# Performance work log

Measured on AMD Instinct MI355X. Metric: run time of the kernel, lower is better.

Reference implementation:

```python
import jax, jax.numpy as jnp
import numpy as np
from math import sqrt

EMA_W = 0.3  # ema_weight
LN_EPS = 1e-5


def setup_inputs() -> dict:
    key = jax.random.key(0)
    ks = jax.random.split(key, 16)
    B, L, H, E = 8, 1024, 8, 64
    d_ff, dp_rank = 2048, 8
    inp = {
        "queries": jax.random.normal(ks[0], (B, L, H, E), jnp.float32),
        "keys": jax.random.normal(ks[1], (B, L, H, E), jnp.float32),
        "values": jax.random.normal(ks[2], (B, L, H, E), jnp.float32),
        "attn_mask": jnp.zeros((B, 1, L, L), jnp.bool_),
        # dynamic-projection mlp: Linear(E, dp_rank)
        "mlp_w": jax.random.normal(ks[3], (E, dp_rank), jnp.float32) / sqrt(E),
        "mlp_b": jnp.zeros((dp_rank,), jnp.float32),
        # ff_1: Linear(E,d_ff) -> GELU -> Linear(d_ff,E)
        "ff1_w1": jax.random.normal(ks[4], (E, d_ff), jnp.float32) / sqrt(E),
        "ff1_b1": jnp.zeros((d_ff,), jnp.float32),
        "ff1_w2": jax.random.normal(ks[5], (d_ff, E), jnp.float32) / sqrt(d_ff),
        "ff1_b2": jnp.zeros((E,), jnp.float32),
        # ff_2
        "ff2_w1": jax.random.normal(ks[6], (E, d_ff), jnp.float32) / sqrt(E),
        "ff2_b1": jnp.zeros((d_ff,), jnp.float32),
        "ff2_w2": jax.random.normal(ks[7], (d_ff, E), jnp.float32) / sqrt(d_ff),
        "ff2_b2": jnp.zeros((E,), jnp.float32),
        # LayerNorm(E)
        "ln_w": jnp.ones((E,), jnp.float32),
        "ln_b": jnp.zeros((E,), jnp.float32),
    }
    return inp


def _dynamic_projection(src, mlp_w, mlp_b):
    # src: [B,L,H,E] -> softmax over dp_rank, then einsum 'blhe,blhr->blhe'
    sm = jax.nn.softmax(src @ mlp_w + mlp_b, axis=-1)  # [B,L,H,R]
    return jnp.einsum('blhe,blhr->blhe', src, sm)


def _ffn(x, w1, b1, w2, b2):
    return jax.nn.gelu(x @ w1 + b1, approximate=False) @ w2 + b2


def reference(queries, keys, values, attn_mask,
              mlp_w, mlp_b,
              ff1_w1, ff1_b1, ff1_w2, ff1_b2,
              ff2_w1, ff2_b1, ff2_w2, ff2_b2,
              ln_w, ln_b):
    E = queries.shape[-1]
    scale = 1.0 / sqrt(24.0)   # hardcoded in source
    scale1 = 1.0 / sqrt(E)

    dp_values = _dynamic_projection(values, mlp_w, mlp_b)
    dp_keys = _dynamic_projection(keys, mlp_w, mlp_b)

    # ema state starts at zeros every forward, so ema = (1-w) * x
    ema_queries = (1.0 - EMA_W) * queries
    ema_keys = (1.0 - EMA_W) * dp_keys

    # NOTE: source masks a scores tensor that is then overwritten; mask has
    # no effect on the output, so attn_mask is unused (kept for fidelity).
    scores = jnp.einsum('blhe,bshe->bhls', ema_queries, ema_keys)
    scores1 = jnp.einsum('blhe,bshe->bhls', queries, keys)

    A = jax.nn.softmax(scale * scores, axis=-1)    # dropout = identity (eval)
    A1 = jax.nn.softmax(scale1 * scores1, axis=-1)

    V = jnp.einsum('bhls,bshd->blhd', A, dp_values)
    V1 = jnp.einsum('bhls,bshd->blhd', A1, values)

    src = _ffn(V, ff1_w1, ff1_b1, ff1_w2, ff1_b2) + _ffn(V1, ff2_w1, ff2_b1, ff2_w2, ff2_b2)

    mu = jnp.mean(src, axis=-1, keepdims=True)
    var = jnp.mean(jnp.square(src - mu), axis=-1, keepdims=True)
    out = (src - mu) * jax.lax.rsqrt(var + LN_EPS) * ln_w + ln_b
    return out
```

## Files before the change

### kernel.cpp

```cpp
#include <hip/hip_runtime.h>

typedef _Float16 f16x8 __attribute__((ext_vector_type(8)));
typedef _Float16 f16x2 __attribute__((ext_vector_type(2)));
typedef float f32x4 __attribute__((ext_vector_type(4)));
typedef float f32x16 __attribute__((ext_vector_type(16)));
typedef unsigned short u16x8 __attribute__((ext_vector_type(8)));
typedef unsigned int u32x4 __attribute__((ext_vector_type(4)));

static __device__ __forceinline__ unsigned short f2h(float x) {
  return __builtin_bit_cast(unsigned short, (_Float16)x);
}
static __device__ __forceinline__ float h2f(unsigned short u) {
  return (float)__builtin_bit_cast(_Float16, u);
}

static __device__ __forceinline__ f16x2 gelu_pk(f16x2 x) {
  const f16x2 P4 = {(_Float16)4.0f, (_Float16)4.0f};
  const f16x2 N4 = {(_Float16)-4.0f, (_Float16)-4.0f};
  const f16x2 C1 = {(_Float16)0.392761f, (_Float16)0.392761f};
  const f16x2 C3 = {(_Float16)-0.0512736f, (_Float16)-0.0512736f};
  const f16x2 C5 = {(_Float16)0.00376322f, (_Float16)0.00376322f};
  const f16x2 C7 = {(_Float16)-0.000100287f, (_Float16)-0.000100287f};
  const f16x2 HF = {(_Float16)0.5f, (_Float16)0.5f};
  const f16x2 ONE = {(_Float16)1.0f, (_Float16)1.0f};
  const f16x2 ZRO = {(_Float16)0.0f, (_Float16)0.0f};
  f16x2 xc = __builtin_elementwise_max(__builtin_elementwise_min(x, P4), N4);
  f16x2 u = xc * xc;
  f16x2 p = __builtin_elementwise_fma(
      __builtin_elementwise_fma(__builtin_elementwise_fma(C7, u, C5), u, C3),
      u, C1);
  f16x2 q = __builtin_elementwise_fma(xc, p, HF);
  f16x2 qc = __builtin_elementwise_max(__builtin_elementwise_min(q, ONE), ZRO);
  return x * qc;
}

static __device__ __forceinline__ int sig16(int v) {
  return (v & ~12) | ((v & 4) << 1) | ((v & 8) >> 1);
}

__global__ __launch_bounds__(256) void k_prep(
    const float* __restrict__ vsrc, const float* __restrict__ ksrc,
    const float* __restrict__ w11, const float* __restrict__ w21,
    const float* __restrict__ w12, const float* __restrict__ w22,
    unsigned short* __restrict__ vtb, unsigned short* __restrict__ kf16,
    unsigned short* __restrict__ w1t1, unsigned short* __restrict__ w2t1,
    unsigned short* __restrict__ w1t2, unsigned short* __restrict__ w2t2) {
  int bid = blockIdx.x, tid = threadIdx.x;
  if (bid >= 1152) {
    int kb = bid - 1152, bh = kb >> 4, lt = kb & 15, b = bh >> 3, h = bh & 7;
    const float* src = ksrc + (((b * 1024 + lt * 64) * 8 + h) << 6);
    unsigned short* dst = kf16 + bh * 65536 + lt * 64 * 64;
#pragma unroll
    for (int i = 0; i < 2; ++i) {
      int c = tid + i * 256, r = c >> 3, c0 = (c & 7) * 8;
      const float* s = src + r * 512 + c0;
      f32x4 a = *(const f32x4*)s, b4 = *(const f32x4*)(s + 4);
      u16x8 vv;
#pragma unroll
      for (int j = 0; j < 4; ++j) { vv[j] = f2h(a[j]); vv[j + 4] = f2h(b4[j]); }
      *(u16x8*)(dst + r * 64 + c0) = vv;
    }
    return;
  }
  __shared__ unsigned short t[64][72];
  const float* src; unsigned short* dst; int srs, drs;
  bool isw2 = false;
  if (bid < 1024) {
    int bh = bid >> 4, lt = bid & 15, b = bh >> 3, h = bh & 7;
    src = vsrc + (((b * 1024 + lt * 64) * 8 + h) << 6); srs = 512;
    dst = vtb + bh * 65536 + lt * 64; drs = 1024;
  } else {
    int wb = bid - 1024, which = wb >> 5, ti = wb & 31;
    isw2 = (which & 1);
    if (which == 0)      { src = w11 + ti * 64;   srs = 2048; dst = w1t1 + ti * 4096; drs = 64; }
    else if (which == 1) { src = w21 + ti * 4096; srs = 64;   dst = w2t1 + ti * 64;   drs = 2048; }
    else if (which == 2) { src = w12 + ti * 64;   srs = 2048; dst = w1t2 + ti * 4096; drs = 64; }
    else                 { src = w22 + ti * 4096; srs = 64;   dst = w2t2 + ti * 64;   drs = 2048; }
  }
#pragma unroll
  for (int i = 0; i < 2; ++i) {
    int c = tid + i * 256, r = c >> 3, c0 = (c & 7) * 8;
    const float* s = src + r * srs + c0;
    int tr = isw2 ? sig16(r) : r;
#pragma unroll
    for (int j = 0; j < 8; ++j) t[c0 + j][tr] = f2h(s[j]);
  }
  __syncthreads();
#pragma unroll
  for (int i = 0; i < 2; ++i) {
    int c = tid + i * 256, r = c >> 3, c0 = (c & 7) * 8;
    u16x8 vv;
#pragma unroll
    for (int j = 0; j < 8; ++j) vv[j] = t[r][c0 + j];
    *(u16x8*)(dst + r * drs + c0) = vv;
  }
}

__global__ __launch_bounds__(64) __attribute__((amdgpu_waves_per_eu(1, 1)))
void k_attn(
    const float* __restrict__ q, const unsigned short* __restrict__ kf16,
    const unsigned short* __restrict__ vtb,
    unsigned short* __restrict__ Vo, unsigned short* __restrict__ V1o) {
  int bid = blockIdx.x;
  int swz = (bid & 7) * 128 + (bid >> 3);
  int bh = swz >> 4, rb = swz & 15;
  int b = bh >> 3, h = bh & 7;
  int lane = threadIdx.x & 63, t = lane & 15, g = lane >> 4;

  __shared__ unsigned short Pl[2][4096];

  f16x8 aq[4][2];
#pragma unroll
  for (int sub = 0; sub < 4; ++sub) {
    int row = rb * 64 + sub * 16 + t;
    const float* qp = q + ((b * 1024 + row) * 8 + h) * 64;
#pragma unroll
    for (int ks = 0; ks < 2; ++ks) {
      f32x4 q0 = *(const f32x4*)(qp + ks * 32 + g * 8);
      f32x4 q1 = *(const f32x4*)(qp + ks * 32 + g * 8 + 4);
      f16x8 a;
#pragma unroll
      for (int j = 0; j < 4; ++j) { a[j] = (_Float16)q0[j]; a[j + 4] = (_Float16)q1[j]; }
      aq[sub][ks] = a;
    }
  }

  const float scl[2] = {0.14429954f, 0.18033688f};
  float lsp[2][4][4];
  f32x4 o[2][4][4];
#pragma unroll
  for (int v = 0; v < 2; ++v)
#pragma unroll
    for (int sub = 0; sub < 4; ++sub)
#pragma unroll
      for (int i = 0; i < 4; ++i) {
        lsp[v][sub][i] = 0.f;
        o[v][sub][i] = (f32x4){0, 0, 0, 0};
      }

  const unsigned short* kfb = kf16 + bh * 65536;
  const unsigned short* vbase = vtb + bh * 65536;

  f16x8 bk[8];
#pragma unroll
  for (int ks = 0; ks < 2; ++ks)
#pragma unroll
    for (int nt = 0; nt < 4; ++nt)
      bk[ks * 4 + nt] = *(const f16x8*)(kfb + (nt * 16 + t) * 64 + (ks * 4 + g) * 8);

#pragma unroll 1
  for (int kt = 0; kt < 16; ++kt) {
    f16x8 bv[8];
#pragma unroll
    for (int ks = 0; ks < 2; ++ks)
#pragma unroll
      for (int nt = 0; nt < 4; ++nt)
        bv[ks * 4 + nt] = *(const f16x8*)(vbase + (nt * 16 + t) * 1024 + kt * 64 + (ks * 4 + g) * 8);

    f32x4 s[4][4];
#pragma unroll
    for (int sub = 0; sub < 4; ++sub)
#pragma unroll
      for (int nt = 0; nt < 4; ++nt) s[sub][nt] = (f32x4){0, 0, 0, 0};
#pragma unroll
    for (int ks = 0; ks < 2; ++ks)
#pragma unroll
      for (int sub = 0; sub < 4; ++sub)
#pragma unroll
        for (int nt = 0; nt < 4; ++nt)
          s[sub][nt] = __builtin_amdgcn_mfma_f32_16x16x32_f16(
              aq[sub][ks], bk[ks * 4 + nt], s[sub][nt], 0, 0, 0);

    if (kt < 15) {
#pragma unroll
      for (int ks = 0; ks < 2; ++ks)
#pragma unroll
        for (int nt = 0; nt < 4; ++nt)
          bk[ks * 4 + nt] = *(const f16x8*)(kfb + ((kt + 1) * 64 + nt * 16 + t) * 64 + (ks * 4 + g) * 8);
    }
    __builtin_amdgcn_sched_barrier(0);

#pragma unroll
    for (int v = 0; v < 2; ++v)
#pragma unroll
      for (int sub = 0; sub < 4; ++sub) {
        float pr[4][4];
#pragma unroll
        for (int nt = 0; nt < 4; ++nt)
#pragma unroll
          for (int reg = 0; reg < 4; ++reg)
            pr[nt][reg] = fminf(exp2f(s[sub][nt][reg] * scl[v]), 60000.0f);
#pragma unroll
        for (int nt = 0; nt < 4; ++nt)
#pragma unroll
          for (int reg = 0; reg < 4; ++reg) {
            int r = g * 4 + reg, sc = nt * 16 + t;
            Pl[v][(sub * 16 + r) * 64 + ((((sc >> 3) ^ (r & 7)) << 3) | (sc & 7))] =
                f2h(pr[nt][reg]);
          }
#pragma unroll
        for (int reg = 0; reg < 4; ++reg)
          lsp[v][sub][reg] += (pr[0][reg] + pr[1][reg]) + (pr[2][reg] + pr[3][reg]);
      }
    asm volatile("s_waitcnt lgkmcnt(0)" ::: "memory");
#pragma unroll
    for (int v = 0; v < 2; ++v)
#pragma unroll
      for (int ks = 0; ks < 2; ++ks)
#pragma unroll
        for (int sub = 0; sub < 4; ++sub) {
          f16x8 ap = *(const f16x8*)&Pl[v][(sub * 16 + t) * 64 +
                                           (((ks * 4 + g) ^ (t & 7)) << 3)];
#pragma unroll
          for (int nt = 0; nt < 4; ++nt)
            o[v][sub][nt] = __builtin_amdgcn_mfma_f32_16x16x32_f16(
                ap, bv[ks * 4 + nt], o[v][sub][nt], 0, 0, 0);
        }
  }

#pragma unroll
  for (int v = 0; v < 2; ++v)
#pragma unroll
    for (int sub = 0; sub < 4; ++sub)
#pragma unroll
      for (int dd = 1; dd < 16; dd <<= 1)
#pragma unroll
        for (int reg = 0; reg < 4; ++reg)
          lsp[v][sub][reg] += __shfl_xor(lsp[v][sub][reg], dd);

#pragma unroll
  for (int sub = 0; sub < 4; ++sub)
#pragma unroll
    for (int nt = 0; nt < 4; ++nt)
#pragma unroll
      for (int reg = 0; reg < 4; ++reg) {
        int row = rb * 64 + sub * 16 + g * 4 + reg;
        int idx = ((b * 1024 + row) * 8 + h) * 64 + nt * 16 + t;
        float r0 = __builtin_amdgcn_rcpf(lsp[0][sub][reg]);
        float r1 = __builtin_amdgcn_rcpf(lsp[1][sub][reg]);
        Vo[idx]  = f2h(o[0][sub][nt][reg] * r0);
        V1o[idx] = f2h(o[1][sub][nt][reg] * r1);
      }
}

static __device__ __forceinline__ void compute_chunk(
    int j, const unsigned short* __restrict__ W1buf,
    const unsigned short* __restrict__ W2buf,
    const float* __restrict__ biasL, const f16x8 (&bx)[4],
    f32x16& acc0, f32x16& acc1, int t5, int hh) {
  f32x16 d0, d1;
#pragma unroll
  for (int rq = 0; rq < 4; ++rq) {
    f32x4 bb0 = *(const f32x4*)(biasL + j * 64 + rq * 8 + hh * 4);
    f32x4 bb1 = *(const f32x4*)(biasL + j * 64 + 32 + rq * 8 + hh * 4);
#pragma unroll
    for (int jj = 0; jj < 4; ++jj) { d0[rq * 4 + jj] = bb0[jj]; d1[rq * 4 + jj] = bb1[jj]; }
  }
#pragma unroll
  for (int ks = 0; ks < 4; ++ks) {
    int fr0 = t5;
    f16x8 aw0 = *(const f16x8*)&W1buf[fr0 * 64 + (((ks * 2 + hh) ^ (fr0 & 7)) << 3)];
    d0 = __builtin_amdgcn_mfma_f32_32x32x16_f16(aw0, bx[ks], d0, 0, 0, 0);
    int fr1 = 32 + t5;
    f16x8 aw1 = *(const f16x8*)&W1buf[fr1 * 64 + (((ks * 2 + hh) ^ (fr1 & 7)) << 3)];
    d1 = __builtin_amdgcn_mfma_f32_32x32x16_f16(aw1, bx[ks], d1, 0, 0, 0);
  }
#pragma unroll
  for (int g = 0; g < 4; ++g) {
    u32x4 av;
#pragma unroll
    for (int q = 0; q < 4; ++q) {
      int base = (g & 1) * 8 + 2 * q;
      float lo = (g < 2) ? d0[base] : d1[base];
      float hi = (g < 2) ? d0[base + 1] : d1[base + 1];
      f16x2 hx = __builtin_bit_cast(f16x2, __builtin_amdgcn_cvt_pkrtz(lo, hi));
      av[q] = __builtin_bit_cast(unsigned, gelu_pk(hx));
    }
    f16x8 hb = __builtin_bit_cast(f16x8, av);
    int er0 = t5;
    f16x8 wa0 = *(const f16x8*)&W2buf[er0 * 64 + (((g * 2 + hh) ^ (er0 & 7)) << 3)];
    acc0 = __builtin_amdgcn_mfma_f32_32x32x16_f16(wa0, hb, acc0, 0, 0, 0);
    int er1 = 32 + t5;
    f16x8 wa1 = *(const f16x8*)&W2buf[er1 * 64 + (((g * 2 + hh) ^ (er1 & 7)) << 3)];
    acc1 = __builtin_amdgcn_mfma_f32_32x32x16_f16(wa1, hb, acc1, 0, 0, 0);
  }
}

__global__ __launch_bounds__(256) void k_ffn(
    const unsigned short* __restrict__ Vo, const unsigned short* __restrict__ V1o,
    const unsigned short* __restrict__ w1ta, const unsigned short* __restrict__ w2ta,
    const unsigned short* __restrict__ w1tb, const unsigned short* __restrict__ w2tb,
    const float* __restrict__ b1a, const float* __restrict__ b1b,
    unsigned short* __restrict__ p0, unsigned short* __restrict__ p1,
    unsigned short* __restrict__ p2, unsigned short* __restrict__ p3) {
  int bid = blockIdx.x;
  int quar = bid >> 9, rb = bid & 511;
  int tid = threadIdx.x, w = tid >> 6, lane = tid & 63;
  int t5 = lane & 31, hh = lane >> 5;
  int rowbase = rb * 128 + w * 32;
  unsigned short* pout = (quar == 0) ? p0 : (quar == 1) ? p1 : (quar == 2) ? p2 : p3;

  __shared__ unsigned short W1c[4096];
  __shared__ unsigned short W2c[4096];
  __shared__ float biasL[2][512];

  if (tid < 128) {
    *(f32x4*)&biasL[0][tid * 4] = *(const f32x4*)(b1a + quar * 512 + tid * 4);
    *(f32x4*)&biasL[1][tid * 4] = *(const f32x4*)(b1b + quar * 512 + tid * 4);
  }

  f32x16 acc0, acc1;
#pragma unroll
  for (int i = 0; i < 16; ++i) { acc0[i] = 0.f; acc1[i] = 0.f; }

  int r0 = tid >> 3, c8 = tid & 7;
  int sw = (c8 ^ (r0 & 7)) << 3;

#pragma unroll 1
  for (int ffn = 0; ffn < 2; ++ffn) {
    const unsigned short* X = ffn ? V1o : Vo;
    const unsigned short* w1t = ffn ? w1tb : w1ta;
    const unsigned short* w2t = ffn ? w2tb : w2ta;
    f16x8 bx[4];
#pragma unroll
    for (int ks = 0; ks < 4; ++ks)
      bx[ks] = *(const f16x8*)(X + (rowbase + t5) * 64 + ks * 16 + hh * 8);

    int cbase = quar * 8;
    u16x8 ra0 = *(const u16x8*)(w1t + (cbase * 64 + r0) * 64 + c8 * 8);
    u16x8 ra1 = *(const u16x8*)(w1t + (cbase * 64 + r0 + 32) * 64 + c8 * 8);
    u16x8 rb0 = *(const u16x8*)(w2t + r0 * 2048 + cbase * 64 + c8 * 8);
    u16x8 rb1 = *(const u16x8*)(w2t + (r0 + 32) * 2048 + cbase * 64 + c8 * 8);

#pragma unroll 1
    for (int j = 0; j < 8; ++j) {
      __syncthreads();
      *(u16x8*)&W1c[r0 * 64 + sw] = ra0;
      *(u16x8*)&W2c[r0 * 64 + sw] = rb0;
      *(u16x8*)&W1c[(r0 + 32) * 64 + sw] = ra1;
      *(u16x8*)&W2c[(r0 + 32) * 64 + sw] = rb1;
      __syncthreads();
      if (j < 7) {
        int c1 = cbase + j + 1;
        ra0 = *(const u16x8*)(w1t + (c1 * 64 + r0) * 64 + c8 * 8);
        ra1 = *(const u16x8*)(w1t + (c1 * 64 + r0 + 32) * 64 + c8 * 8);
        rb0 = *(const u16x8*)(w2t + r0 * 2048 + c1 * 64 + c8 * 8);
        rb1 = *(const u16x8*)(w2t + (r0 + 32) * 2048 + c1 * 64 + c8 * 8);
      }
      compute_chunk(j, W1c, W2c, &biasL[ffn][0], bx, acc0, acc1, t5, hh);
    }
  }

  int orow = rowbase + t5;
#pragma unroll
  for (int q = 0; q < 8; ++q) {
    int e0 = (2 * q & 3) + 8 * (q >> 1) + 4 * hh;
    unsigned pa = __builtin_bit_cast(unsigned,
        __builtin_amdgcn_cvt_pkrtz(acc0[2 * q], acc0[2 * q + 1]));
    unsigned pb = __builtin_bit_cast(unsigned,
        __builtin_amdgcn_cvt_pkrtz(acc1[2 * q], acc1[2 * q + 1]));
    *(unsigned*)(pout + orow * 64 + e0) = pa;
    *(unsigned*)(pout + orow * 64 + 32 + e0) = pb;
  }
}

__global__ __launch_bounds__(256) void k_reduce(
    const unsigned short* __restrict__ p0, const unsigned short* __restrict__ p1,
    const unsigned short* __restrict__ p2, const unsigned short* __restrict__ p3,
    const float* __restrict__ b2a, const float* __restrict__ b2b,
    const float* __restrict__ lnw, const float* __restrict__ lnb,
    float* __restrict__ out) {
  int tid = threadIdx.x, w = tid >> 6, lane = tid & 63;
  float bias = b2a[lane] + b2b[lane];
  float lw = lnw[lane], lb = lnb[lane];
  int wid = blockIdx.x * 4 + w;
#pragma unroll 4
  for (int i = 0; i < 16; ++i) {
    int r = wid * 16 + i;
    int ix = r * 64 + lane;
    float v = (h2f(p0[ix]) + h2f(p1[ix])) + (h2f(p2[ix]) + h2f(p3[ix])) + bias;
    float s1 = v, s2 = v * v;
#pragma unroll
    for (int dd = 1; dd < 64; dd <<= 1) {
      s1 += __shfl_xor(s1, dd);
      s2 += __shfl_xor(s2, dd);
    }
    float mu = s1 * 0.015625f;
    float var = s2 * 0.015625f - mu * mu;
    out[ix] = (v - mu) * rsqrtf(var + 1e-5f) * lw + lb;
  }
}

extern "C" void kernel_launch(void* const* d_in, const int* in_sizes, int n_in,
                              void* d_out, int out_size, void* d_ws, size_t ws_size,
                              hipStream_t stream) {
  (void)in_sizes; (void)n_in; (void)out_size; (void)ws_size;
  const float* q   = (const float*)d_in[0];
  const float* k   = (const float*)d_in[1];
  const float* v   = (const float*)d_in[2];
  const float* w11 = (const float*)d_in[6];
  const float* b11 = (const float*)d_in[7];
  const float* w21 = (const float*)d_in[8];
  const float* b21 = (const float*)d_in[9];
  const float* w12 = (const float*)d_in[10];
  const float* b12 = (const float*)d_in[11];
  const float* w22 = (const float*)d_in[12];
  const float* b22 = (const float*)d_in[13];
  const float* lnw = (const float*)d_in[14];
  const float* lnb = (const float*)d_in[15];

  unsigned short* vtb  = (unsigned short*)d_ws;
  unsigned short* Vo   = vtb + 4194304;
  unsigned short* V1o  = Vo + 4194304;
  unsigned short* w1t1 = V1o + 4194304;
  unsigned short* w2t1 = w1t1 + 131072;
  unsigned short* w1t2 = w2t1 + 131072;
  unsigned short* w2t2 = w1t2 + 131072;
  unsigned short* part1 = w2t2 + 131072;
  unsigned short* kf16  = part1 + 4194304;
  unsigned short* part3 = kf16 + 4194304;
  unsigned short* part0 = vtb;
  unsigned short* part2 = kf16;

  k_prep<<<dim3(2176), dim3(256), 0, stream>>>(v, k, w11, w21, w12, w22,
                                               vtb, kf16, w1t1, w2t1, w1t2, w2t2);
  k_attn<<<dim3(1024), dim3(64), 0, stream>>>(q, kf16, vtb, Vo, V1o);
  k_ffn<<<dim3(2048), dim3(256), 0, stream>>>(Vo, V1o, w1t1, w2t1, w1t2, w2t2,
                                              b11, b12, part0, part1, part2, part3);
  k_reduce<<<dim3(1024), dim3(256), 0, stream>>>(part0, part1, part2, part3,
                                                 b21, b22, lnw, lnb, (float*)d_out);
}
```

Baseline: 216.3 us.

## Pre-swizzle K and V tiles into MFMA fragment order for coalesced loads

The prep kernel now writes the fp16 K and transposed V tiles in per-fragment order, so each 64-lane wave's f16x8 operand load is one contiguous 1KB read at lane*8 instead of a strided gather. This is meant to cut memory transactions and address arithmetic in the attention inner loop. It also relaxes the attention kernel's waves-per-EU hint from 1 to up to 2, which may allow more occupancy but tightens the register budget and can cause spills.

```diff
diff --git a/kernel.cpp b/kernel.cpp
--- a/kernel.cpp
+++ b/kernel.cpp
@@ -49,26 +49,27 @@
   if (bid >= 1152) {
     int kb = bid - 1152, bh = kb >> 4, lt = kb & 15, b = bh >> 3, h = bh & 7;
     const float* src = ksrc + (((b * 1024 + lt * 64) * 8 + h) << 6);
-    unsigned short* dst = kf16 + bh * 65536 + lt * 64 * 64;
+    unsigned short* dst = kf16 + bh * 65536 + lt * 4096;
 #pragma unroll
     for (int i = 0; i < 2; ++i) {
-      int c = tid + i * 256, r = c >> 3, c0 = (c & 7) * 8;
-      const float* s = src + r * 512 + c0;
+      int c = tid + i * 256, r = c >> 3, c8 = c & 7;
+      const float* s = src + r * 512 + c8 * 8;
       f32x4 a = *(const f32x4*)s, b4 = *(const f32x4*)(s + 4);
       u16x8 vv;
 #pragma unroll
       for (int j = 0; j < 4; ++j) { vv[j] = f2h(a[j]); vv[j + 4] = f2h(b4[j]); }
-      *(u16x8*)(dst + r * 64 + c0) = vv;
+      int off = ((c8 >> 2) * 4 + (r >> 4)) * 512 + ((c8 & 3) * 16 + (r & 15)) * 8;
+      *(u16x8*)(dst + off) = vv;
     }
     return;
   }
   __shared__ unsigned short t[64][72];
-  const float* src; unsigned short* dst; int srs, drs;
-  bool isw2 = false;
+  const float* src; unsigned short* dst; int srs, drs = 0;
+  bool isw2 = false, isv = false;
   if (bid < 1024) {
     int bh = bid >> 4, lt = bid & 15, b = bh >> 3, h = bh & 7;
     src = vsrc + (((b * 1024 + lt * 64) * 8 + h) << 6); srs = 512;
-    dst = vtb + bh * 65536 + lt * 64; drs = 1024;
+    dst = vtb + bh * 65536 + lt * 4096; isv = true;
   } else {
     int wb = bid - 1024, which = wb >> 5, ti = wb & 31;
     isw2 = (which & 1);
@@ -88,15 +89,17 @@
   __syncthreads();
 #pragma unroll
   for (int i = 0; i < 2; ++i) {
-    int c = tid + i * 256, r = c >> 3, c0 = (c & 7) * 8;
+    int c = tid + i * 256, r = c >> 3, c8 = c & 7;
     u16x8 vv;
 #pragma unroll
-    for (int j = 0; j < 8; ++j) vv[j] = t[r][c0 + j];
-    *(u16x8*)(dst + r * drs + c0) = vv;
-  }
-}
-
-__global__ __launch_bounds__(64) __attribute__((amdgpu_waves_per_eu(1, 1)))
+    for (int j = 0; j < 8; ++j) vv[j] = t[r][c8 * 8 + j];
+    int off = isv ? ((c8 >> 2) * 4 + (r >> 4)) * 512 + ((c8 & 3) * 16 + (r & 15)) * 8
+                  : r * drs + c8 * 8;
+    *(u16x8*)(dst + off) = vv;
+  }
+}
+
+__global__ __launch_bounds__(64) __attribute__((amdgpu_waves_per_eu(1, 2)))
 void k_attn(
     const float* __restrict__ q, const unsigned short* __restrict__ kf16,
     const unsigned short* __restrict__ vtb,
@@ -143,19 +146,15 @@
 
   f16x8 bk[8];
 #pragma unroll
-  for (int ks = 0; ks < 2; ++ks)
-#pragma unroll
-    for (int nt = 0; nt < 4; ++nt)
-      bk[ks * 4 + nt] = *(const f16x8*)(kfb + (nt * 16 + t) * 64 + (ks * 4 + g) * 8);
+  for (int fr = 0; fr < 8; ++fr)
+    bk[fr] = *(const f16x8*)(kfb + fr * 512 + lane * 8);
 
 #pragma unroll 1
   for (int kt = 0; kt < 16; ++kt) {
     f16x8 bv[8];
 #pragma unroll
-    for (int ks = 0; ks < 2; ++ks)
-#pragma unroll
-      for (int nt = 0; nt < 4; ++nt)
-        bv[ks * 4 + nt] = *(const f16x8*)(vbase + (nt * 16 + t) * 1024 + kt * 64 + (ks * 4 + g) * 8);
+    for (int fr = 0; fr < 8; ++fr)
+      bv[fr] = *(const f16x8*)(vbase + kt * 4096 + fr * 512 + lane * 8);
 
     f32x4 s[4][4];
 #pragma unroll
@@ -173,10 +172,8 @@
 
     if (kt < 15) {
 #pragma unroll
-      for (int ks = 0; ks < 2; ++ks)
-#pragma unroll
-        for (int nt = 0; nt < 4; ++nt)
-          bk[ks * 4 + nt] = *(const f16x8*)(kfb + ((kt + 1) * 64 + nt * 16 + t) * 64 + (ks * 4 + g) * 8);
+      for (int fr = 0; fr < 8; ++fr)
+        bk[fr] = *(const f16x8*)(kfb + (kt + 1) * 4096 + fr * 512 + lane * 8);
     }
     __builtin_amdgcn_sched_barrier(0);
 
```

After: 218.5 us. Within noise of the previous version (+1.0%).
